# Kernel tuning notes

Hardware: AMD Instinct MI355X
Metric: run time of the kernel (lower is better)

The kernel has to match this reference:

```python
import jax, jax.numpy as jnp
import numpy as np

N = 10000      # nodes
E = 160000     # edges (before self-loops)
IN = 128       # input channels
H1, C1 = 8, 128   # layer-1 heads / per-head channels
OUT = 64       # output channels
NEG_SLOPE = 0.2   # PyG GATConv leaky_relu slope


def _glorot(key, shape):
    fan = shape[0] + shape[-1]
    return jax.random.normal(key, shape, jnp.float32) * np.float32(np.sqrt(2.0 / fan))


def setup_inputs() -> dict:
    key = jax.random.key(0)
    ks = jax.random.split(key, 10)
    x = jax.random.normal(ks[0], (N, IN), jnp.float32)
    edge_index = jax.random.randint(ks[1], (2, E), 0, N, dtype=jnp.int64)
    return {
        "x": x,
        "edge_index": edge_index,
        "W1": _glorot(ks[2], (IN, H1 * C1)),
        "a_src1": _glorot(ks[3], (H1, C1)),
        "a_dst1": _glorot(ks[4], (H1, C1)),
        "b1": jnp.zeros((H1 * C1,), jnp.float32),
        "W2": _glorot(ks[5], (H1 * C1, OUT)),
        "a_src2": _glorot(ks[6], (1, OUT)),
        "a_dst2": _glorot(ks[7], (1, OUT)),
        "b2": jnp.zeros((OUT,), jnp.float32),
    }


def gat_conv(x, src, dst, W, a_src, a_dst, bias, heads, ch, concat):
    n = x.shape[0]
    h = (x @ W).reshape(n, heads, ch)                 # [N,H,C]
    alpha_s = jnp.sum(h * a_src, axis=-1)             # [N,H]
    alpha_d = jnp.sum(h * a_dst, axis=-1)             # [N,H]
    e = jax.nn.leaky_relu(alpha_s[src] + alpha_d[dst], NEG_SLOPE)  # [E',H]
    # segment softmax over incoming edges of each dst node
    m = jax.ops.segment_max(e, dst, num_segments=n)
    e = jnp.exp(e - m[dst])
    s = jax.ops.segment_sum(e, dst, num_segments=n)
    alpha = e / (s[dst] + 1e-16)                      # [E',H]
    msg = h[src] * alpha[:, :, None]                  # [E',H,C]
    out = jax.ops.segment_sum(msg, dst, num_segments=n)  # [N,H,C]
    out = out.reshape(n, heads * ch) if concat else jnp.mean(out, axis=1)
    return out + bias


def reference(x, edge_index, W1, a_src1, a_dst1, b1, W2, a_src2, a_dst2, b2):
    n = x.shape[0]
    loops = jnp.arange(n, dtype=edge_index.dtype)     # PyG add_self_loops=True
    src = jnp.concatenate([edge_index[0], loops])
    dst = jnp.concatenate([edge_index[1], loops])
    h = jax.nn.elu(gat_conv(x, src, dst, W1, a_src1, a_dst1, b1, H1, C1, True))
    # dropout is identity in eval mode
    return gat_conv(h, src, dst, W2, a_src2, a_dst2, b2, 1, OUT, False)
```

## Files before the change

### kernel.cpp

```cpp
#include <hip/hip_runtime.h>
#include <math.h>


#define NEG_SLOPE 0.2f

typedef short bf16x8 __attribute__((ext_vector_type(8)));
typedef float f32x4 __attribute__((ext_vector_type(4)));

__device__ __forceinline__ float leaky(float v) { return v >= 0.0f ? v : NEG_SLOPE * v; }

__device__ __forceinline__ unsigned short f2bf(float f) {
    unsigned u = __float_as_uint(f);
    u += 0x7FFFu + ((u >> 16) & 1u);
    return (unsigned short)(u >> 16);
}


__global__ __launch_bounds__(256) void init_k(
    const float* __restrict__ W1, const float* __restrict__ a_src1,
    const float* __restrict__ a_dst1,
    float* __restrict__ As_t, float* __restrict__ Ad_t,
    int* __restrict__ counts, int N) {
    int b = blockIdx.x;
    int nzb = (N + 255) >> 8;
    if (b < nzb) {
        int i = b * 256 + threadIdx.x;
        if (i < N) counts[i] = 0;
    } else {
        int i = (b - nzb) * 256 + threadIdx.x;
        int k = i >> 3, h = i & 7;
        float ss = 0.f, sd = 0.f;
        for (int c = 0; c < 128; c += 4) {
            float4 w = *(const float4*)(W1 + (size_t)k * 1024 + h * 128 + c);
            float4 a = *(const float4*)(a_src1 + h * 128 + c);
            float4 d = *(const float4*)(a_dst1 + h * 128 + c);
            ss += w.x * a.x + w.y * a.y + w.z * a.z + w.w * a.w;
            sd += w.x * d.x + w.y * d.y + w.z * d.z + w.w * d.w;
        }
        As_t[h * 132 + k] = ss;
        Ad_t[h * 132 + k] = sd;
    }
}


__global__ __launch_bounds__(1024) void alpha_k(
    const float* __restrict__ x, const float* __restrict__ As_t, const float* __restrict__ Ad_t,
    float* __restrict__ as1, float* __restrict__ ad1, int N) {
    int t = threadIdx.x;
    __shared__ float sAs[1056], sAd[1056];
    for (int i = t; i < 1056; i += 1024) {
        sAs[i] = As_t[i];
        sAd[i] = Ad_t[i];
    }
    __syncthreads();
    int node = blockIdx.x * 128 + (t >> 3);
    int h = t & 7;
    if (node >= N) return;
    const float* sa = sAs + h * 132;
    const float* sd = sAd + h * 132;
    float accs = 0.f, accd = 0.f;
    for (int k = 0; k < 128; k += 4) {
        float4 xv = *(const float4*)(x + (size_t)node * 128 + k);
        float4 av = *(const float4*)(sa + k);
        float4 dv = *(const float4*)(sd + k);
        accs += xv.x * av.x + xv.y * av.y + xv.z * av.z + xv.w * av.w;
        accd += xv.x * dv.x + xv.y * dv.y + xv.z * dv.z + xv.w * dv.w;
    }
    as1[node * 8 + h] = accs;
    ad1[node * 8 + h] = accd;
}


__global__ __launch_bounds__(256) void fill_plus(
    const int* __restrict__ ei, int* __restrict__ counts,
    const float* __restrict__ as1, const float* __restrict__ ad1,
    const float* __restrict__ W1, const float* __restrict__ W2,
    int* __restrict__ srcs, float* __restrict__ wbuf,
    unsigned short* __restrict__ W1bT, unsigned short* __restrict__ W2bT,
    int E, int N) {
    int M = E + N;
    int nb_count = (M + 255) >> 8;
    int b = blockIdx.x;
    if (b < nb_count) {
        int i = b * 256 + threadIdx.x;
        if (i >= M) return;
        int src, dst;
        if (i < E) { src = ei[i]; dst = ei[E + i]; }
        else       { src = dst = i - E; }
        int slot = atomicAdd(&counts[dst], 1);
        if (slot < 64) {
            int pos = dst * 64 + slot;
            srcs[pos] = src;
            float4 a0 = *(const float4*)(as1 + (size_t)src * 8);
            float4 a1 = *(const float4*)(as1 + (size_t)src * 8 + 4);
            float4 b0 = *(const float4*)(ad1 + (size_t)dst * 8);
            float4 b1 = *(const float4*)(ad1 + (size_t)dst * 8 + 4);
            float4 w0, w1;
            w0.x = __expf(leaky(a0.x + b0.x));
            w0.y = __expf(leaky(a0.y + b0.y));
            w0.z = __expf(leaky(a0.z + b0.z));
            w0.w = __expf(leaky(a0.w + b0.w));
            w1.x = __expf(leaky(a1.x + b1.x));
            w1.y = __expf(leaky(a1.y + b1.y));
            w1.z = __expf(leaky(a1.z + b1.z));
            w1.w = __expf(leaky(a1.w + b1.w));
            *(float4*)(wbuf + (size_t)pos * 8)     = w0;
            *(float4*)(wbuf + (size_t)pos * 8 + 4) = w1;
        }
        return;
    }
    __shared__ unsigned short tile[32][33];
    int bb = b - nb_count;
    if (bb < 128) {
        int kt = bb & 3, hct = bb >> 2;
        int j = threadIdx.x & 31;
        int i0 = threadIdx.x >> 5;
        for (int i = i0; i < 32; i += 8)
            tile[i][j] = f2bf(W1[(size_t)(kt * 32 + i) * 1024 + hct * 32 + j]);
        __syncthreads();
        for (int i = i0; i < 32; i += 8) {
            int hc = hct * 32 + i, k = kt * 32 + j;
            int h = hc >> 7, c = hc & 127;
            W1bT[h * 16384 + c * 128 + k] = tile[j][i];
        }
    } else {
        bb -= 128;
        int kt = bb & 31, ctile = bb >> 5;
        int j = threadIdx.x & 31;
        int i0 = threadIdx.x >> 5;
        for (int i = i0; i < 32; i += 8)
            tile[i][j] = f2bf(W2[(size_t)(kt * 32 + i) * 64 + ctile * 32 + j]);
        __syncthreads();
        for (int i = i0; i < 32; i += 8)
            W2bT[(size_t)(ctile * 32 + i) * 1024 + kt * 32 + j] = tile[j][i];
    }
}


__global__ __launch_bounds__(256) void l1_gather(
    const float* __restrict__ x, const float* __restrict__ wbuf,
    const int* __restrict__ counts, const int* __restrict__ srcs,
    unsigned short* __restrict__ y_b, int N) {
    int n = blockIdx.x * 4 + (threadIdx.x >> 6);
    if (n >= N) return;
    int lane = threadIdx.x & 63;
    int beg = n * 64;
    int deg = counts[n];
    deg = deg < 64 ? deg : 64;
    float2 acc[8];
#pragma unroll
    for (int h = 0; h < 8; h++) acc[h] = make_float2(0.f, 0.f);
    float4 ws0 = make_float4(0.f, 0.f, 0.f, 0.f);
    float4 ws1 = make_float4(0.f, 0.f, 0.f, 0.f);
    const float* xb = x + lane * 2;
#define L1G_BODY(EIDX, SRC)                                                      \
    {                                                                            \
        float4 w0_ = *(const float4*)(wbuf + (size_t)(EIDX) * 8);                \
        float4 w1_ = *(const float4*)(wbuf + (size_t)(EIDX) * 8 + 4);            \
        float2 xv_ = *(const float2*)(xb + (size_t)(SRC) * 128);                 \
        ws0.x += w0_.x; ws0.y += w0_.y; ws0.z += w0_.z; ws0.w += w0_.w;          \
        ws1.x += w1_.x; ws1.y += w1_.y; ws1.z += w1_.z; ws1.w += w1_.w;          \
        acc[0].x = fmaf(w0_.x, xv_.x, acc[0].x); acc[0].y = fmaf(w0_.x, xv_.y, acc[0].y); \
        acc[1].x = fmaf(w0_.y, xv_.x, acc[1].x); acc[1].y = fmaf(w0_.y, xv_.y, acc[1].y); \
        acc[2].x = fmaf(w0_.z, xv_.x, acc[2].x); acc[2].y = fmaf(w0_.z, xv_.y, acc[2].y); \
        acc[3].x = fmaf(w0_.w, xv_.x, acc[3].x); acc[3].y = fmaf(w0_.w, xv_.y, acc[3].y); \
        acc[4].x = fmaf(w1_.x, xv_.x, acc[4].x); acc[4].y = fmaf(w1_.x, xv_.y, acc[4].y); \
        acc[5].x = fmaf(w1_.y, xv_.x, acc[5].x); acc[5].y = fmaf(w1_.y, xv_.y, acc[5].y); \
        acc[6].x = fmaf(w1_.z, xv_.x, acc[6].x); acc[6].y = fmaf(w1_.z, xv_.y, acc[6].y); \
        acc[7].x = fmaf(w1_.w, xv_.x, acc[7].x); acc[7].y = fmaf(w1_.w, xv_.y, acc[7].y); \
    }
    int sv = srcs[beg + (lane < deg ? lane : 0)];
    int i = 0;
    for (; i + 4 <= deg; i += 4) {
        int s0 = __shfl(sv, i);
        int s1 = __shfl(sv, i + 1);
        int s2 = __shfl(sv, i + 2);
        int s3 = __shfl(sv, i + 3);
        L1G_BODY(beg + i, s0)
        L1G_BODY(beg + i + 1, s1)
        L1G_BODY(beg + i + 2, s2)
        L1G_BODY(beg + i + 3, s3)
    }
    for (; i < deg; i++) {
        int s = __shfl(sv, i);
        L1G_BODY(beg + i, s)
    }
#undef L1G_BODY
    float inv[8] = {1.f / (ws0.x + 1e-16f), 1.f / (ws0.y + 1e-16f),
                    1.f / (ws0.z + 1e-16f), 1.f / (ws0.w + 1e-16f),
                    1.f / (ws1.x + 1e-16f), 1.f / (ws1.y + 1e-16f),
                    1.f / (ws1.z + 1e-16f), 1.f / (ws1.w + 1e-16f)};
    unsigned short* dst = y_b + (size_t)n * 1024 + lane * 2;
#pragma unroll
    for (int h = 0; h < 8; h++) {
        unsigned lo = f2bf(acc[h].x * inv[h]);
        unsigned hi = f2bf(acc[h].y * inv[h]);
        *(unsigned*)(dst + h * 128) = lo | (hi << 16);
    }
}


__global__ __launch_bounds__(256) void l12_gemm(
    const unsigned short* __restrict__ y_b, const unsigned short* __restrict__ W1bT,
    const float* __restrict__ b1, const unsigned short* __restrict__ W2bT,
    const float* __restrict__ a_src2, const float* __restrict__ a_dst2,
    float* __restrict__ h2, float* __restrict__ as2, float* __restrict__ ad2, int N) {
    int nb = blockIdx.x * 16;
    int w = threadIdx.x >> 6;
    int lane = threadIdx.x & 63;
    int n16 = lane & 15, quad = lane >> 4;
    __shared__ unsigned short hb[16 * 1032];
    __shared__ float sA[4][16], sD[4][16];
    int node_a = nb + n16;
    const unsigned short* yrow = y_b + (size_t)(node_a < N ? node_a : 0) * 1024;
#pragma unroll
    for (int cti = 0; cti < 16; cti++) {
        int ct = w * 16 + cti;
        int h = ct >> 3;
        int cc = (ct & 7) * 16;
        const unsigned short* Wh = W1bT + h * 16384 + (size_t)(cc + n16) * 128 + quad * 8;
        const unsigned short* ya = yrow + h * 128 + quad * 8;
        f32x4 acc = (f32x4){0.f, 0.f, 0.f, 0.f};
#pragma unroll
        for (int ks = 0; ks < 4; ks++) {
            bf16x8 a = *(const bf16x8*)(ya + ks * 32);
            bf16x8 b = *(const bf16x8*)(Wh + ks * 32);
            acc = __builtin_amdgcn_mfma_f32_16x16x32_bf16(a, b, acc, 0, 0, 0);
        }
        int c = h * 128 + cc + n16;
        float bias = b1[c];
#pragma unroll
        for (int r = 0; r < 4; r++) {
            float v = acc[r] + bias;
            v = v > 0.f ? v : expm1f(v);
            hb[(quad * 4 + r) * 1032 + c] = f2bf(v);
        }
    }
    __syncthreads();
    const unsigned short* arow = hb + n16 * 1032 + quad * 8;
    const unsigned short* brow = W2bT + (size_t)(w * 16 + n16) * 1024 + quad * 8;
    f32x4 acc = (f32x4){0.f, 0.f, 0.f, 0.f};
#pragma unroll 8
    for (int ks = 0; ks < 32; ks++) {
        bf16x8 a = *(const bf16x8*)(arow + ks * 32);
        bf16x8 b = *(const bf16x8*)(brow + ks * 32);
        acc = __builtin_amdgcn_mfma_f32_16x16x32_bf16(a, b, acc, 0, 0, 0);
    }
    int c2 = w * 16 + n16;
    float asc = a_src2[c2], adc = a_dst2[c2];
    float pav[4], pdv[4];
#pragma unroll
    for (int r = 0; r < 4; r++) {
        int node = nb + quad * 4 + r;
        if (node < N) h2[(size_t)node * 64 + c2] = acc[r];
        pav[r] = acc[r] * asc;
        pdv[r] = acc[r] * adc;
#pragma unroll
        for (int mm = 1; mm <= 8; mm <<= 1) {
            pav[r] += __shfl_xor(pav[r], mm);
            pdv[r] += __shfl_xor(pdv[r], mm);
        }
    }
    if (n16 == 0) {
#pragma unroll
        for (int r = 0; r < 4; r++) {
            sA[w][quad * 4 + r] = pav[r];
            sD[w][quad * 4 + r] = pdv[r];
        }
    }
    __syncthreads();
    if (threadIdx.x < 16) {
        int node = nb + threadIdx.x;
        if (node < N) {
            as2[node] = sA[0][threadIdx.x] + sA[1][threadIdx.x] + sA[2][threadIdx.x] + sA[3][threadIdx.x];
            ad2[node] = sD[0][threadIdx.x] + sD[1][threadIdx.x] + sD[2][threadIdx.x] + sD[3][threadIdx.x];
        }
    }
}


__global__ __launch_bounds__(256) void l2_gather(
    const float* __restrict__ h2, const float* __restrict__ as2,
    const float* __restrict__ ad2, const float* __restrict__ b2,
    const int* __restrict__ counts, const int* __restrict__ srcs,
    float* __restrict__ out, int N) {
    int n = blockIdx.x * 4 + (threadIdx.x >> 6);
    if (n >= N) return;
    int lane = threadIdx.x & 63;
    int beg = n * 64;
    int deg = counts[n];
    deg = deg < 64 ? deg : 64;
    float adn = ad2[n];
    float acc = 0.f;
    int sv = srcs[beg + (lane < deg ? lane : 0)];
    float wv = (lane < deg) ? __expf(leaky(as2[sv] + adn)) : 0.f;
    int i = 0;
    for (; i + 4 <= deg; i += 4) {
        int s0 = __shfl(sv, i),     s1 = __shfl(sv, i + 1);
        int s2 = __shfl(sv, i + 2), s3 = __shfl(sv, i + 3);
        float w0 = __shfl(wv, i),     w1 = __shfl(wv, i + 1);
        float w2 = __shfl(wv, i + 2), w3 = __shfl(wv, i + 3);
        float v0 = h2[(size_t)s0 * 64 + lane];
        float v1 = h2[(size_t)s1 * 64 + lane];
        float v2 = h2[(size_t)s2 * 64 + lane];
        float v3 = h2[(size_t)s3 * 64 + lane];
        acc = fmaf(w0, v0, acc);
        acc = fmaf(w1, v1, acc);
        acc = fmaf(w2, v2, acc);
        acc = fmaf(w3, v3, acc);
    }
    for (; i < deg; i++) {
        int s = __shfl(sv, i);
        float ww = __shfl(wv, i);
        acc = fmaf(ww, h2[(size_t)s * 64 + lane], acc);
    }
    float wsum = wv;
#pragma unroll
    for (int mm = 1; mm <= 32; mm <<= 1) wsum += __shfl_xor(wsum, mm);
    out[(size_t)n * 64 + lane] = acc / (wsum + 1e-16f) + b2[lane];
}


static inline size_t align_up(size_t v, size_t a) { return (v + a - 1) / a * a; }

extern "C" void kernel_launch(void* const* d_in, const int* in_sizes, int n_in,
                              void* d_out, int out_size, void* d_ws, size_t ws_size,
                              hipStream_t stream) {
    const float* x      = (const float*)d_in[0];
    const int*   ei     = (const int*)d_in[1];
    const float* W1     = (const float*)d_in[2];
    const float* a_src1 = (const float*)d_in[3];
    const float* a_dst1 = (const float*)d_in[4];
    const float* b1     = (const float*)d_in[5];
    const float* W2     = (const float*)d_in[6];
    const float* a_src2 = (const float*)d_in[7];
    const float* a_dst2 = (const float*)d_in[8];
    const float* b2     = (const float*)d_in[9];
    float* out = (float*)d_out;

    int N = in_sizes[0] / 128;
    int E = in_sizes[1] / 2;
    int M = E + N;

    char* p = (char*)d_ws;
    size_t off = 0;
    auto carve = [&](size_t bytes) {
        void* r = p + off;
        off = align_up(off + bytes, 256);
        return r;
    };
    int*            counts  = (int*)carve((size_t)N * 4);
    int*            srcs    = (int*)carve((size_t)N * 64 * 4);
    float*          As_t    = (float*)carve(1056 * 4);
    float*          Ad_t    = (float*)carve(1056 * 4);
    float*          as1     = (float*)carve((size_t)N * 8 * 4);
    float*          ad1     = (float*)carve((size_t)N * 8 * 4);
    float*          as2     = (float*)carve((size_t)N * 4);
    float*          ad2     = (float*)carve((size_t)N * 4);
    float*          h2      = (float*)carve((size_t)N * 64 * 4);
    float*          wbuf    = (float*)carve((size_t)N * 64 * 8 * 4);
    unsigned short* W1bT    = (unsigned short*)carve((size_t)8 * 128 * 128 * 2);
    unsigned short* W2bT    = (unsigned short*)carve((size_t)64 * 1024 * 2);
    unsigned short* y_b     = (unsigned short*)carve((size_t)N * 1024 * 2);
    (void)ws_size;

    int nzb      = (N + 255) / 256;
    int nb_alpha = (N + 127) / 128;
    int nb_count = (M + 255) / 256;

    init_k<<<nzb + 4, 256, 0, stream>>>(W1, a_src1, a_dst1, As_t, Ad_t, counts, N);
    alpha_k<<<nb_alpha, 1024, 0, stream>>>(x, As_t, Ad_t, as1, ad1, N);
    fill_plus<<<nb_count + 192, 256, 0, stream>>>(ei, counts, as1, ad1, W1, W2,
                                                  srcs, wbuf, W1bT, W2bT, E, N);
    l1_gather<<<(N + 3) / 4, 256, 0, stream>>>(x, wbuf, counts, srcs, y_b, N);
    l12_gemm<<<(N + 15) / 16, 256, 0, stream>>>(y_b, W1bT, b1, W2bT, a_src2, a_dst2,
                                                h2, as2, ad2, N);
    l2_gather<<<(N + 3) / 4, 256, 0, stream>>>(h2, as2, ad2, b2, counts, srcs, out, N);
}
```

Measured before the change: 180.1 us.

## Fuse init into alpha kernel and unroll gathers by eight with masking

Removes the separate init kernel by having every alpha_k block recompute the W1·a projections into shared memory and zero counts with a grid-stride loop, saving one launch and a global round trip. Each block now redoes the 128x8 projection (1024 threads, each reading 128 W1 floats), which is redundant work across about 79 blocks. The l1 and l2 gather loops now run in fully unrolled groups of eight edges, padded and masked to zero weight, replacing the unroll-by-4 plus remainder loop. This gives more memory-level parallelism but does extra loads for the padded edges.

New measurement: 223.9 us. 1.24x slower.

```diff
diff --git a/kernel.cpp b/kernel.cpp
--- a/kernel.cpp
+++ b/kernel.cpp
@@ -16,19 +16,16 @@
 }
 
 
-__global__ __launch_bounds__(256) void init_k(
-    const float* __restrict__ W1, const float* __restrict__ a_src1,
-    const float* __restrict__ a_dst1,
-    float* __restrict__ As_t, float* __restrict__ Ad_t,
+__global__ __launch_bounds__(1024) void alpha_k(
+    const float* __restrict__ x, const float* __restrict__ W1,
+    const float* __restrict__ a_src1, const float* __restrict__ a_dst1,
+    float* __restrict__ as1, float* __restrict__ ad1,
     int* __restrict__ counts, int N) {
-    int b = blockIdx.x;
-    int nzb = (N + 255) >> 8;
-    if (b < nzb) {
-        int i = b * 256 + threadIdx.x;
-        if (i < N) counts[i] = 0;
-    } else {
-        int i = (b - nzb) * 256 + threadIdx.x;
-        int k = i >> 3, h = i & 7;
+    int t = threadIdx.x;
+    for (int i = blockIdx.x * 1024 + t; i < N; i += gridDim.x * 1024) counts[i] = 0;
+    __shared__ float sAs[1056], sAd[1056];
+    {
+        int k = t >> 3, h = t & 7;
         float ss = 0.f, sd = 0.f;
         for (int c = 0; c < 128; c += 4) {
             float4 w = *(const float4*)(W1 + (size_t)k * 1024 + h * 128 + c);
@@ -37,20 +34,8 @@
             ss += w.x * a.x + w.y * a.y + w.z * a.z + w.w * a.w;
             sd += w.x * d.x + w.y * d.y + w.z * d.z + w.w * d.w;
         }
-        As_t[h * 132 + k] = ss;
-        Ad_t[h * 132 + k] = sd;
-    }
-}
-
-
-__global__ __launch_bounds__(1024) void alpha_k(
-    const float* __restrict__ x, const float* __restrict__ As_t, const float* __restrict__ Ad_t,
-    float* __restrict__ as1, float* __restrict__ ad1, int N) {
-    int t = threadIdx.x;
-    __shared__ float sAs[1056], sAd[1056];
-    for (int i = t; i < 1056; i += 1024) {
-        sAs[i] = As_t[i];
-        sAd[i] = Ad_t[i];
+        sAs[h * 132 + k] = ss;
+        sAd[h * 132 + k] = sd;
     }
     __syncthreads();
     int node = blockIdx.x * 128 + (t >> 3);
@@ -147,45 +132,39 @@
     int beg = n * 64;
     int deg = counts[n];
     deg = deg < 64 ? deg : 64;
+    int deg8 = (deg + 7) & ~7;
     float2 acc[8];
 #pragma unroll
     for (int h = 0; h < 8; h++) acc[h] = make_float2(0.f, 0.f);
     float4 ws0 = make_float4(0.f, 0.f, 0.f, 0.f);
     float4 ws1 = make_float4(0.f, 0.f, 0.f, 0.f);
     const float* xb = x + lane * 2;
-#define L1G_BODY(EIDX, SRC)                                                      \
-    {                                                                            \
-        float4 w0_ = *(const float4*)(wbuf + (size_t)(EIDX) * 8);                \
-        float4 w1_ = *(const float4*)(wbuf + (size_t)(EIDX) * 8 + 4);            \
-        float2 xv_ = *(const float2*)(xb + (size_t)(SRC) * 128);                 \
-        ws0.x += w0_.x; ws0.y += w0_.y; ws0.z += w0_.z; ws0.w += w0_.w;          \
-        ws1.x += w1_.x; ws1.y += w1_.y; ws1.z += w1_.z; ws1.w += w1_.w;          \
-        acc[0].x = fmaf(w0_.x, xv_.x, acc[0].x); acc[0].y = fmaf(w0_.x, xv_.y, acc[0].y); \
-        acc[1].x = fmaf(w0_.y, xv_.x, acc[1].x); acc[1].y = fmaf(w0_.y, xv_.y, acc[1].y); \
-        acc[2].x = fmaf(w0_.z, xv_.x, acc[2].x); acc[2].y = fmaf(w0_.z, xv_.y, acc[2].y); \
-        acc[3].x = fmaf(w0_.w, xv_.x, acc[3].x); acc[3].y = fmaf(w0_.w, xv_.y, acc[3].y); \
-        acc[4].x = fmaf(w1_.x, xv_.x, acc[4].x); acc[4].y = fmaf(w1_.x, xv_.y, acc[4].y); \
-        acc[5].x = fmaf(w1_.y, xv_.x, acc[5].x); acc[5].y = fmaf(w1_.y, xv_.y, acc[5].y); \
-        acc[6].x = fmaf(w1_.z, xv_.x, acc[6].x); acc[6].y = fmaf(w1_.z, xv_.y, acc[6].y); \
-        acc[7].x = fmaf(w1_.w, xv_.x, acc[7].x); acc[7].y = fmaf(w1_.w, xv_.y, acc[7].y); \
-    }
     int sv = srcs[beg + (lane < deg ? lane : 0)];
-    int i = 0;
-    for (; i + 4 <= deg; i += 4) {
-        int s0 = __shfl(sv, i);
-        int s1 = __shfl(sv, i + 1);
-        int s2 = __shfl(sv, i + 2);
-        int s3 = __shfl(sv, i + 3);
-        L1G_BODY(beg + i, s0)
-        L1G_BODY(beg + i + 1, s1)
-        L1G_BODY(beg + i + 2, s2)
-        L1G_BODY(beg + i + 3, s3)
-    }
-    for (; i < deg; i++) {
-        int s = __shfl(sv, i);
-        L1G_BODY(beg + i, s)
-    }
-#undef L1G_BODY
+    for (int i = 0; i < deg8; i += 8) {
+#pragma unroll
+        for (int j = 0; j < 8; j++) {
+            int e = i + j;
+            int s_ = __shfl(sv, e);
+            float4 w0_ = *(const float4*)(wbuf + (size_t)(beg + e) * 8);
+            float4 w1_ = *(const float4*)(wbuf + (size_t)(beg + e) * 8 + 4);
+            bool v_ = e < deg;
+            w0_.x = v_ ? w0_.x : 0.f; w0_.y = v_ ? w0_.y : 0.f;
+            w0_.z = v_ ? w0_.z : 0.f; w0_.w = v_ ? w0_.w : 0.f;
+            w1_.x = v_ ? w1_.x : 0.f; w1_.y = v_ ? w1_.y : 0.f;
+            w1_.z = v_ ? w1_.z : 0.f; w1_.w = v_ ? w1_.w : 0.f;
+            float2 xv_ = *(const float2*)(xb + (size_t)s_ * 128);
+            ws0.x += w0_.x; ws0.y += w0_.y; ws0.z += w0_.z; ws0.w += w0_.w;
+            ws1.x += w1_.x; ws1.y += w1_.y; ws1.z += w1_.z; ws1.w += w1_.w;
+            acc[0].x = fmaf(w0_.x, xv_.x, acc[0].x); acc[0].y = fmaf(w0_.x, xv_.y, acc[0].y);
+            acc[1].x = fmaf(w0_.y, xv_.x, acc[1].x); acc[1].y = fmaf(w0_.y, xv_.y, acc[1].y);
+            acc[2].x = fmaf(w0_.z, xv_.x, acc[2].x); acc[2].y = fmaf(w0_.z, xv_.y, acc[2].y);
+            acc[3].x = fmaf(w0_.w, xv_.x, acc[3].x); acc[3].y = fmaf(w0_.w, xv_.y, acc[3].y);
+            acc[4].x = fmaf(w1_.x, xv_.x, acc[4].x); acc[4].y = fmaf(w1_.x, xv_.y, acc[4].y);
+            acc[5].x = fmaf(w1_.y, xv_.x, acc[5].x); acc[5].y = fmaf(w1_.y, xv_.y, acc[5].y);
+            acc[6].x = fmaf(w1_.z, xv_.x, acc[6].x); acc[6].y = fmaf(w1_.z, xv_.y, acc[6].y);
+            acc[7].x = fmaf(w1_.w, xv_.x, acc[7].x); acc[7].y = fmaf(w1_.w, xv_.y, acc[7].y);
+        }
+    }
     float inv[8] = {1.f / (ws0.x + 1e-16f), 1.f / (ws0.y + 1e-16f),
                     1.f / (ws0.z + 1e-16f), 1.f / (ws0.w + 1e-16f),
                     1.f / (ws1.x + 1e-16f), 1.f / (ws1.y + 1e-16f),
@@ -290,29 +269,19 @@
     int beg = n * 64;
     int deg = counts[n];
     deg = deg < 64 ? deg : 64;
+    int deg8 = (deg + 7) & ~7;
     float adn = ad2[n];
     float acc = 0.f;
     int sv = srcs[beg + (lane < deg ? lane : 0)];
     float wv = (lane < deg) ? __expf(leaky(as2[sv] + adn)) : 0.f;
-    int i = 0;
-    for (; i + 4 <= deg; i += 4) {
-        int s0 = __shfl(sv, i),     s1 = __shfl(sv, i + 1);
-        int s2 = __shfl(sv, i + 2), s3 = __shfl(sv, i + 3);
-        float w0 = __shfl(wv, i),     w1 = __shfl(wv, i + 1);
-        float w2 = __shfl(wv, i + 2), w3 = __shfl(wv, i + 3);
-        float v0 = h2[(size_t)s0 * 64 + lane];
-        float v1 = h2[(size_t)s1 * 64 + lane];
-        float v2 = h2[(size_t)s2 * 64 + lane];
-        float v3 = h2[(size_t)s3 * 64 + lane];
-        acc = fmaf(w0, v0, acc);
-        acc = fmaf(w1, v1, acc);
-        acc = fmaf(w2, v2, acc);
-        acc = fmaf(w3, v3, acc);
-    }
-    for (; i < deg; i++) {
-        int s = __shfl(sv, i);
-        float ww = __shfl(wv, i);
-        acc = fmaf(ww, h2[(size_t)s * 64 + lane], acc);
+    for (int i = 0; i < deg8; i += 8) {
+#pragma unroll
+        for (int j = 0; j < 8; j++) {
+            int e = i + j;
+            int s_ = __shfl(sv, e);
+            float w_ = __shfl(wv, e);
+            acc = fmaf(w_, h2[(size_t)s_ * 64 + lane], acc);
+        }
     }
     float wsum = wv;
 #pragma unroll
@@ -351,8 +320,6 @@
     };
     int*            counts  = (int*)carve((size_t)N * 4);
     int*            srcs    = (int*)carve((size_t)N * 64 * 4);
-    float*          As_t    = (float*)carve(1056 * 4);
-    float*          Ad_t    = (float*)carve(1056 * 4);
     float*          as1     = (float*)carve((size_t)N * 8 * 4);
     float*          ad1     = (float*)carve((size_t)N * 8 * 4);
     float*          as2     = (float*)carve((size_t)N * 4);
@@ -364,12 +331,10 @@
     unsigned short* y_b     = (unsigned short*)carve((size_t)N * 1024 * 2);
     (void)ws_size;
 
-    int nzb      = (N + 255) / 256;
     int nb_alpha = (N + 127) / 128;
     int nb_count = (M + 255) / 256;
 
-    init_k<<<nzb + 4, 256, 0, stream>>>(W1, a_src1, a_dst1, As_t, Ad_t, counts, N);
-    alpha_k<<<nb_alpha, 1024, 0, stream>>>(x, As_t, Ad_t, as1, ad1, N);
+    alpha_k<<<nb_alpha, 1024, 0, stream>>>(x, W1, a_src1, a_dst1, as1, ad1, counts, N);
     fill_plus<<<nb_count + 192, 256, 0, stream>>>(ei, counts, as1, ad1, W1, W2,
                                                   srcs, wbuf, W1bT, W2bT, E, N);
     l1_gather<<<(N + 3) / 4, 256, 0, stream>>>(x, wbuf, counts, srcs, y_b, N);
```

## Compute edge attention weights in gather via LDS, merge fill with alpha kernel

Applied to the files above, without the earlier changes.

The edge-weight exp computation moves out of the CSR fill kernel into l1_gather, where each wave computes the weights for its node's edges into shared memory, so the N*64*8 float wbuf is never written to or read from global memory. Because the fill no longer needs as1/ad1, it is merged into the alpha kernel as independent blocks, and the W1/W2 bf16 transposes move into init_k, cutting one kernel launch. This adds LDS usage and some redundant loads of as1 per source in the gather.

Result: faster. 162.2 us (median of 2 runs) (-9.9%).

```diff
diff --git a/kernel.cpp b/kernel.cpp
--- a/kernel.cpp
+++ b/kernel.cpp
@@ -18,16 +18,20 @@
 
 __global__ __launch_bounds__(256) void init_k(
     const float* __restrict__ W1, const float* __restrict__ a_src1,
-    const float* __restrict__ a_dst1,
+    const float* __restrict__ a_dst1, const float* __restrict__ W2,
     float* __restrict__ As_t, float* __restrict__ Ad_t,
+    unsigned short* __restrict__ W1bT, unsigned short* __restrict__ W2bT,
     int* __restrict__ counts, int N) {
     int b = blockIdx.x;
     int nzb = (N + 255) >> 8;
     if (b < nzb) {
         int i = b * 256 + threadIdx.x;
         if (i < N) counts[i] = 0;
-    } else {
-        int i = (b - nzb) * 256 + threadIdx.x;
+        return;
+    }
+    b -= nzb;
+    if (b < 4) {
+        int i = b * 256 + threadIdx.x;
         int k = i >> 3, h = i & 7;
         float ss = 0.f, sd = 0.f;
         for (int c = 0; c < 128; c += 4) {
@@ -39,62 +43,96 @@
         }
         As_t[h * 132 + k] = ss;
         Ad_t[h * 132 + k] = sd;
-    }
-}
-
-
-__global__ __launch_bounds__(1024) void alpha_k(
+        return;
+    }
+    b -= 4;
+    __shared__ unsigned short tile[32][33];
+    if (b < 128) {
+        int kt = b & 3, hct = b >> 2;
+        int j = threadIdx.x & 31;
+        int i0 = threadIdx.x >> 5;
+        for (int i = i0; i < 32; i += 8)
+            tile[i][j] = f2bf(W1[(size_t)(kt * 32 + i) * 1024 + hct * 32 + j]);
+        __syncthreads();
+        for (int i = i0; i < 32; i += 8) {
+            int hc = hct * 32 + i, k = kt * 32 + j;
+            int h = hc >> 7, c = hc & 127;
+            W1bT[h * 16384 + c * 128 + k] = tile[j][i];
+        }
+    } else {
+        b -= 128;
+        int kt = b & 31, ctile = b >> 5;
+        int j = threadIdx.x & 31;
+        int i0 = threadIdx.x >> 5;
+        for (int i = i0; i < 32; i += 8)
+            tile[i][j] = f2bf(W2[(size_t)(kt * 32 + i) * 64 + ctile * 32 + j]);
+        __syncthreads();
+        for (int i = i0; i < 32; i += 8)
+            W2bT[(size_t)(ctile * 32 + i) * 1024 + kt * 32 + j] = tile[j][i];
+    }
+}
+
+
+__global__ __launch_bounds__(1024) void alpha_fill(
     const float* __restrict__ x, const float* __restrict__ As_t, const float* __restrict__ Ad_t,
-    float* __restrict__ as1, float* __restrict__ ad1, int N) {
+    const int* __restrict__ ei, int* __restrict__ counts,
+    float* __restrict__ as1, float* __restrict__ ad1,
+    int* __restrict__ srcs, int E, int N, int nb_alpha) {
     int t = threadIdx.x;
-    __shared__ float sAs[1056], sAd[1056];
-    for (int i = t; i < 1056; i += 1024) {
-        sAs[i] = As_t[i];
-        sAd[i] = Ad_t[i];
-    }
-    __syncthreads();
-    int node = blockIdx.x * 128 + (t >> 3);
-    int h = t & 7;
-    if (node >= N) return;
-    const float* sa = sAs + h * 132;
-    const float* sd = sAd + h * 132;
-    float accs = 0.f, accd = 0.f;
-    for (int k = 0; k < 128; k += 4) {
-        float4 xv = *(const float4*)(x + (size_t)node * 128 + k);
-        float4 av = *(const float4*)(sa + k);
-        float4 dv = *(const float4*)(sd + k);
-        accs += xv.x * av.x + xv.y * av.y + xv.z * av.z + xv.w * av.w;
-        accd += xv.x * dv.x + xv.y * dv.y + xv.z * dv.z + xv.w * dv.w;
-    }
-    as1[node * 8 + h] = accs;
-    ad1[node * 8 + h] = accd;
-}
-
-
-__global__ __launch_bounds__(256) void fill_plus(
-    const int* __restrict__ ei, int* __restrict__ counts,
-    const float* __restrict__ as1, const float* __restrict__ ad1,
-    const float* __restrict__ W1, const float* __restrict__ W2,
-    int* __restrict__ srcs, float* __restrict__ wbuf,
-    unsigned short* __restrict__ W1bT, unsigned short* __restrict__ W2bT,
-    int E, int N) {
-    int M = E + N;
-    int nb_count = (M + 255) >> 8;
-    int b = blockIdx.x;
-    if (b < nb_count) {
-        int i = b * 256 + threadIdx.x;
+    if ((int)blockIdx.x < nb_alpha) {
+        __shared__ float sAs[1056], sAd[1056];
+        for (int i = t; i < 1056; i += 1024) {
+            sAs[i] = As_t[i];
+            sAd[i] = Ad_t[i];
+        }
+        __syncthreads();
+        int node = blockIdx.x * 128 + (t >> 3);
+        int h = t & 7;
+        if (node >= N) return;
+        const float* sa = sAs + h * 132;
+        const float* sd = sAd + h * 132;
+        float accs = 0.f, accd = 0.f;
+        for (int k = 0; k < 128; k += 4) {
+            float4 xv = *(const float4*)(x + (size_t)node * 128 + k);
+            float4 av = *(const float4*)(sa + k);
+            float4 dv = *(const float4*)(sd + k);
+            accs += xv.x * av.x + xv.y * av.y + xv.z * av.z + xv.w * av.w;
+            accd += xv.x * dv.x + xv.y * dv.y + xv.z * dv.z + xv.w * dv.w;
+        }
+        as1[node * 8 + h] = accs;
+        ad1[node * 8 + h] = accd;
+    } else {
+        int i = ((int)blockIdx.x - nb_alpha) * 1024 + t;
+        int M = E + N;
         if (i >= M) return;
         int src, dst;
         if (i < E) { src = ei[i]; dst = ei[E + i]; }
         else       { src = dst = i - E; }
         int slot = atomicAdd(&counts[dst], 1);
-        if (slot < 64) {
-            int pos = dst * 64 + slot;
-            srcs[pos] = src;
-            float4 a0 = *(const float4*)(as1 + (size_t)src * 8);
-            float4 a1 = *(const float4*)(as1 + (size_t)src * 8 + 4);
-            float4 b0 = *(const float4*)(ad1 + (size_t)dst * 8);
-            float4 b1 = *(const float4*)(ad1 + (size_t)dst * 8 + 4);
+        if (slot < 64) srcs[dst * 64 + slot] = src;
+    }
+}
+
+
+__global__ __launch_bounds__(256) void l1_gather(
+    const float* __restrict__ x, const float* __restrict__ as1,
+    const float* __restrict__ ad1, const int* __restrict__ counts,
+    const int* __restrict__ srcs, unsigned short* __restrict__ y_b, int N) {
+    int wid = threadIdx.x >> 6;
+    int n = blockIdx.x * 4 + wid;
+    if (n >= N) return;
+    int lane = threadIdx.x & 63;
+    int beg = n * 64;
+    int deg = counts[n];
+    deg = deg < 64 ? deg : 64;
+    __shared__ float wls[4][64][8];
+    int sv = srcs[beg + (lane < deg ? lane : 0)];
+    {
+        float4 a0 = *(const float4*)(as1 + (size_t)sv * 8);
+        float4 a1 = *(const float4*)(as1 + (size_t)sv * 8 + 4);
+        float4 b0 = *(const float4*)(ad1 + (size_t)n * 8);
+        float4 b1 = *(const float4*)(ad1 + (size_t)n * 8 + 4);
+        if (lane < deg) {
             float4 w0, w1;
             w0.x = __expf(leaky(a0.x + b0.x));
             w0.y = __expf(leaky(a0.y + b0.y));
@@ -104,59 +142,20 @@
             w1.y = __expf(leaky(a1.y + b1.y));
             w1.z = __expf(leaky(a1.z + b1.z));
             w1.w = __expf(leaky(a1.w + b1.w));
-            *(float4*)(wbuf + (size_t)pos * 8)     = w0;
-            *(float4*)(wbuf + (size_t)pos * 8 + 4) = w1;
-        }
-        return;
-    }
-    __shared__ unsigned short tile[32][33];
-    int bb = b - nb_count;
-    if (bb < 128) {
-        int kt = bb & 3, hct = bb >> 2;
-        int j = threadIdx.x & 31;
-        int i0 = threadIdx.x >> 5;
-        for (int i = i0; i < 32; i += 8)
-            tile[i][j] = f2bf(W1[(size_t)(kt * 32 + i) * 1024 + hct * 32 + j]);
-        __syncthreads();
-        for (int i = i0; i < 32; i += 8) {
-            int hc = hct * 32 + i, k = kt * 32 + j;
-            int h = hc >> 7, c = hc & 127;
-            W1bT[h * 16384 + c * 128 + k] = tile[j][i];
-        }
-    } else {
-        bb -= 128;
-        int kt = bb & 31, ctile = bb >> 5;
-        int j = threadIdx.x & 31;
-        int i0 = threadIdx.x >> 5;
-        for (int i = i0; i < 32; i += 8)
-            tile[i][j] = f2bf(W2[(size_t)(kt * 32 + i) * 64 + ctile * 32 + j]);
-        __syncthreads();
-        for (int i = i0; i < 32; i += 8)
-            W2bT[(size_t)(ctile * 32 + i) * 1024 + kt * 32 + j] = tile[j][i];
-    }
-}
-
-
-__global__ __launch_bounds__(256) void l1_gather(
-    const float* __restrict__ x, const float* __restrict__ wbuf,
-    const int* __restrict__ counts, const int* __restrict__ srcs,
-    unsigned short* __restrict__ y_b, int N) {
-    int n = blockIdx.x * 4 + (threadIdx.x >> 6);
-    if (n >= N) return;
-    int lane = threadIdx.x & 63;
-    int beg = n * 64;
-    int deg = counts[n];
-    deg = deg < 64 ? deg : 64;
+            *(float4*)&wls[wid][lane][0] = w0;
+            *(float4*)&wls[wid][lane][4] = w1;
+        }
+    }
     float2 acc[8];
 #pragma unroll
     for (int h = 0; h < 8; h++) acc[h] = make_float2(0.f, 0.f);
     float4 ws0 = make_float4(0.f, 0.f, 0.f, 0.f);
     float4 ws1 = make_float4(0.f, 0.f, 0.f, 0.f);
     const float* xb = x + lane * 2;
-#define L1G_BODY(EIDX, SRC)                                                      \
+#define L1G_BODY(E_, SRC)                                                        \
     {                                                                            \
-        float4 w0_ = *(const float4*)(wbuf + (size_t)(EIDX) * 8);                \
-        float4 w1_ = *(const float4*)(wbuf + (size_t)(EIDX) * 8 + 4);            \
+        float4 w0_ = *(const float4*)&wls[wid][E_][0];                           \
+        float4 w1_ = *(const float4*)&wls[wid][E_][4];                           \
         float2 xv_ = *(const float2*)(xb + (size_t)(SRC) * 128);                 \
         ws0.x += w0_.x; ws0.y += w0_.y; ws0.z += w0_.z; ws0.w += w0_.w;          \
         ws1.x += w1_.x; ws1.y += w1_.y; ws1.z += w1_.z; ws1.w += w1_.w;          \
@@ -169,21 +168,20 @@
         acc[6].x = fmaf(w1_.z, xv_.x, acc[6].x); acc[6].y = fmaf(w1_.z, xv_.y, acc[6].y); \
         acc[7].x = fmaf(w1_.w, xv_.x, acc[7].x); acc[7].y = fmaf(w1_.w, xv_.y, acc[7].y); \
     }
-    int sv = srcs[beg + (lane < deg ? lane : 0)];
     int i = 0;
     for (; i + 4 <= deg; i += 4) {
         int s0 = __shfl(sv, i);
         int s1 = __shfl(sv, i + 1);
         int s2 = __shfl(sv, i + 2);
         int s3 = __shfl(sv, i + 3);
-        L1G_BODY(beg + i, s0)
-        L1G_BODY(beg + i + 1, s1)
-        L1G_BODY(beg + i + 2, s2)
-        L1G_BODY(beg + i + 3, s3)
+        L1G_BODY(i, s0)
+        L1G_BODY(i + 1, s1)
+        L1G_BODY(i + 2, s2)
+        L1G_BODY(i + 3, s3)
     }
     for (; i < deg; i++) {
         int s = __shfl(sv, i);
-        L1G_BODY(beg + i, s)
+        L1G_BODY(i, s)
     }
 #undef L1G_BODY
     float inv[8] = {1.f / (ws0.x + 1e-16f), 1.f / (ws0.y + 1e-16f),
@@ -358,7 +356,6 @@
     float*          as2     = (float*)carve((size_t)N * 4);
     float*          ad2     = (float*)carve((size_t)N * 4);
     float*          h2      = (float*)carve((size_t)N * 64 * 4);
-    float*          wbuf    = (float*)carve((size_t)N * 64 * 8 * 4);
     unsigned short* W1bT    = (unsigned short*)carve((size_t)8 * 128 * 128 * 2);
     unsigned short* W2bT    = (unsigned short*)carve((size_t)64 * 1024 * 2);
     unsigned short* y_b     = (unsigned short*)carve((size_t)N * 1024 * 2);
@@ -366,13 +363,13 @@
 
     int nzb      = (N + 255) / 256;
     int nb_alpha = (N + 127) / 128;
-    int nb_count = (M + 255) / 256;
-
-    init_k<<<nzb + 4, 256, 0, stream>>>(W1, a_src1, a_dst1, As_t, Ad_t, counts, N);
-    alpha_k<<<nb_alpha, 1024, 0, stream>>>(x, As_t, Ad_t, as1, ad1, N);
-    fill_plus<<<nb_count + 192, 256, 0, stream>>>(ei, counts, as1, ad1, W1, W2,
-                                                  srcs, wbuf, W1bT, W2bT, E, N);
-    l1_gather<<<(N + 3) / 4, 256, 0, stream>>>(x, wbuf, counts, srcs, y_b, N);
+    int nb_fill  = (M + 1023) / 1024;
+
+    init_k<<<nzb + 4 + 192, 256, 0, stream>>>(W1, a_src1, a_dst1, W2,
+                                              As_t, Ad_t, W1bT, W2bT, counts, N);
+    alpha_fill<<<nb_alpha + nb_fill, 1024, 0, stream>>>(x, As_t, Ad_t, ei, counts,
+                                                        as1, ad1, srcs, E, N, nb_alpha);
+    l1_gather<<<(N + 3) / 4, 256, 0, stream>>>(x, as1, ad1, counts, srcs, y_b, N);
     l12_gemm<<<(N + 15) / 16, 256, 0, stream>>>(y_b, W1bT, b1, W2bT, a_src2, a_dst2,
                                                 h2, as2, ad2, N);
     l2_gather<<<(N + 3) / 4, 256, 0, stream>>>(h2, as2, ad2, b2, counts, srcs, out, N);
```
